# Optimization experiments

Measured on AMD Instinct MI355X. Metric: run time of the kernel, lower is better.

## Reference

```python
import jax, jax.numpy as jnp
import numpy as np

B, S, E = 2, 2048, 2048
H, D = 16, 128
I = 8192
EPS = 1e-5


def layernorm(x, w, b):
    mu = jnp.mean(x, axis=-1, keepdims=True)
    var = jnp.mean(jnp.square(x - mu), axis=-1, keepdims=True)
    return (x - mu) * jax.lax.rsqrt(var + EPS) * w + b


def setup_inputs() -> dict:
    key = jax.random.key(0)
    ks = jax.random.split(key, 6)
    s = 0.02
    return {
        "x": jax.random.normal(ks[0], (B, S, E), jnp.float32),
        "ln1_w": jnp.ones((E,), jnp.float32),
        "ln1_b": jnp.zeros((E,), jnp.float32),
        "Wqkv": jax.random.normal(ks[1], (E, 3 * E), jnp.float32) * s,
        "Wo": jax.random.normal(ks[2], (E, E), jnp.float32) * s,
        "ln2_w": jnp.ones((E,), jnp.float32),
        "ln2_b": jnp.zeros((E,), jnp.float32),
        "W1": jax.random.normal(ks[3], (E, I), jnp.float32) * s,
        "W2": jax.random.normal(ks[4], (I, E), jnp.float32) * s,
    }


def reference(x, ln1_w, ln1_b, Wqkv, Wo, ln2_w, ln2_b, W1, W2):
    scale = D ** -0.5
    # --- attention sublayer (pre-LN) ---
    h = layernorm(x, ln1_w, ln1_b)
    qkv = (h @ Wqkv).reshape(B, S, 3, H, D)
    q, k, v = [jnp.moveaxis(qkv[:, :, i], 1, 2) for i in range(3)]  # [B,H,S,D]
    scores = jnp.einsum("bhqd,bhkd->bhqk", q, k) * scale
    causal = jnp.triu(jnp.ones((S, S), bool), k=1)
    scores = jnp.where(causal, -jnp.inf, scores)
    attn = jax.nn.softmax(scores, axis=-1)
    out = jnp.einsum("bhqk,bhkd->bqhd", attn, v).reshape(B, S, E)
    x = x + out @ Wo
    # --- FFN sublayer (pre-LN) ---
    h = layernorm(x, ln2_w, ln2_b)
    x = x + jax.nn.gelu(h @ W1, approximate=True) @ W2
    return x
```

## Files before the change

kernel.cpp:

```cpp
#include <hip/hip_runtime.h>
#include <hip/hip_bf16.h>

#define B_ 2
#define S_ 2048
#define E_ 2048
#define H_ 16
#define D_ 128
#define I_ 8192
#define T_ (B_*S_)

typedef __attribute__((ext_vector_type(8))) short bf16x8;
typedef __attribute__((ext_vector_type(8))) unsigned short us8;
typedef __attribute__((ext_vector_type(4))) float f32x4;

__device__ __forceinline__ unsigned short f2bf(float f) {
  union { float f; unsigned int u; } c; c.f = f;
  unsigned int u = c.u;
  unsigned int r = (u + 0x7fffu + ((u >> 16) & 1u)) >> 16;
  return (unsigned short)r;
}

__device__ __forceinline__ void gload16(const void* g, void* l) {
  __builtin_amdgcn_global_load_lds((const __attribute__((address_space(1))) void*)g,
                                   (__attribute__((address_space(3))) void*)l, 16, 0, 0);
}

__global__ void transpose_w(const float* __restrict__ in, unsigned short* __restrict__ out,
                            int K, int N) {
  __shared__ float tile[32][33];
  const int n0 = blockIdx.x * 32, k0 = blockIdx.y * 32;
  const int tx = threadIdx.x, ty = threadIdx.y;
#pragma unroll
  for (int j = 0; j < 4; ++j) {
    int k = k0 + ty + j * 8;
    tile[ty + j * 8][tx] = in[(size_t)k * N + n0 + tx];
  }
  __syncthreads();
#pragma unroll
  for (int j = 0; j < 4; ++j) {
    int n = n0 + ty + j * 8;
    out[(size_t)n * K + k0 + tx] = f2bf(tile[tx][ty + j * 8]);
  }
}

__global__ void ln_kernel(const float* __restrict__ x, const float* __restrict__ w,
                          const float* __restrict__ b, unsigned short* __restrict__ out) {
  const int row = blockIdx.x;
  const int tid = threadIdx.x;
  const int wid = tid >> 6, lane = tid & 63;
  const float4* xr = (const float4*)(x + (size_t)row * E_);
  float4 v0 = xr[tid * 2], v1 = xr[tid * 2 + 1];
  float s  = v0.x + v0.y + v0.z + v0.w + v1.x + v1.y + v1.z + v1.w;
  float sq = v0.x*v0.x + v0.y*v0.y + v0.z*v0.z + v0.w*v0.w
           + v1.x*v1.x + v1.y*v1.y + v1.z*v1.z + v1.w*v1.w;
#pragma unroll
  for (int off = 32; off > 0; off >>= 1) {
    s  += __shfl_xor(s, off);
    sq += __shfl_xor(sq, off);
  }
  __shared__ float red[8];
  if (lane == 0) { red[wid] = s; red[wid + 4] = sq; }
  __syncthreads();
  s  = red[0] + red[1] + red[2] + red[3];
  sq = red[4] + red[5] + red[6] + red[7];
  const float mu  = s * (1.0f / E_);
  const float var = sq * (1.0f / E_) - mu * mu;
  const float rstd = rsqrtf(var + 1e-5f);
  const float4* w4 = (const float4*)w + tid * 2;
  const float4* b4 = (const float4*)b + tid * 2;
  float4 w0 = w4[0], w1 = w4[1], bb0 = b4[0], bb1 = b4[1];
  us8 o;
  o[0] = f2bf((v0.x - mu) * rstd * w0.x + bb0.x);
  o[1] = f2bf((v0.y - mu) * rstd * w0.y + bb0.y);
  o[2] = f2bf((v0.z - mu) * rstd * w0.z + bb0.z);
  o[3] = f2bf((v0.w - mu) * rstd * w0.w + bb0.w);
  o[4] = f2bf((v1.x - mu) * rstd * w1.x + bb1.x);
  o[5] = f2bf((v1.y - mu) * rstd * w1.y + bb1.y);
  o[6] = f2bf((v1.z - mu) * rstd * w1.z + bb1.z);
  o[7] = f2bf((v1.w - mu) * rstd * w1.w + bb1.w);
  *(us8*)(&out[(size_t)row * E_ + tid * 8]) = o;
}

template<int EPI>
__global__ void gemm_bt(const unsigned short* __restrict__ A,
                        const unsigned short* __restrict__ Bt,
                        void* __restrict__ Cout,
                        const float* __restrict__ resid,
                        int M, int N, int K) {
  __shared__ __align__(16) unsigned short As[128 * 32];
  __shared__ __align__(16) unsigned short Bs[128 * 32];
  const int gn = N >> 7;
  const int nwg = (M >> 7) * gn;
  const int cpx = nwg >> 3;
  const int bid = blockIdx.x;
  const int swz = (bid & 7) * cpx + (bid >> 3);
  const int bm = swz / gn, bn = swz % gn;
  const int tid = threadIdx.x;
  const int wid = tid >> 6, lane = tid & 63;
  const int fr = lane & 15, kg = lane >> 4;
  const int wr = wid >> 1, wc = wid & 1;

  const int c0 = wid * 2;
  const unsigned short* gA = A  + (size_t)(bm * 128 + c0 * 16 + (lane >> 2)) * K + (lane & 3) * 8;
  const unsigned short* gB = Bt + (size_t)(bn * 128 + c0 * 16 + (lane >> 2)) * K + (lane & 3) * 8;
  unsigned short* lA = &As[c0 * 512];
  unsigned short* lB = &Bs[c0 * 512];

  const unsigned short* rA = &As[(wr * 64 + fr) * 32 + kg * 8];
  const unsigned short* rB = &Bs[(wc * 64 + fr) * 32 + kg * 8];

  f32x4 acc[4][4] = {};
  const int nk = K >> 5;
  for (int kt = 0; kt < nk; ++kt) {
    __syncthreads();
    gload16(gA,                 lA);
    gload16(gA + 16 * (size_t)K, lA + 512);
    gload16(gB,                 lB);
    gload16(gB + 16 * (size_t)K, lB + 512);
    gA += 32; gB += 32;
    __syncthreads();
    bf16x8 af[4], bfr[4];
#pragma unroll
    for (int m = 0; m < 4; ++m) af[m]  = *(const bf16x8*)(rA + m * 16 * 32);
#pragma unroll
    for (int n = 0; n < 4; ++n) bfr[n] = *(const bf16x8*)(rB + n * 16 * 32);
#pragma unroll
    for (int m = 0; m < 4; ++m)
#pragma unroll
      for (int n = 0; n < 4; ++n)
        acc[m][n] = __builtin_amdgcn_mfma_f32_16x16x32_bf16(af[m], bfr[n], acc[m][n], 0, 0, 0);
  }

  const int row0 = bm * 128 + wr * 64;
  const int col0 = bn * 128 + wc * 64;
#pragma unroll
  for (int m = 0; m < 4; ++m) {
#pragma unroll
    for (int n = 0; n < 4; ++n) {
#pragma unroll
      for (int r = 0; r < 4; ++r) {
        const int row = row0 + m * 16 + kg * 4 + r;
        const int col = col0 + n * 16 + fr;
        const size_t idx = (size_t)row * N + col;
        const float v = acc[m][n][r];
        if constexpr (EPI == 0) {
          ((unsigned short*)Cout)[idx] = f2bf(v);
        } else if constexpr (EPI == 1) {
          const float u = 0.7978845608028654f * (v + 0.044715f * v * v * v);
          const float gel = 0.5f * v * (1.0f + tanhf(u));
          ((unsigned short*)Cout)[idx] = f2bf(gel);
        } else {
          ((float*)Cout)[idx] = v + resid[idx];
        }
      }
    }
  }
}

__global__ void extract_vT(const unsigned short* __restrict__ qkv, unsigned short* __restrict__ vT) {
  __shared__ unsigned short tile[32][34];
  const int bh = blockIdx.z;
  const int b = bh >> 4, h = bh & 15;
  const int s0 = blockIdx.y * 32, d0 = blockIdx.x * 32;
  const int tx = threadIdx.x, ty = threadIdx.y;
#pragma unroll
  for (int j = 0; j < 4; ++j) {
    int s = s0 + ty + j * 8;
    tile[ty + j * 8][tx] = qkv[(size_t)(b * S_ + s) * 6144 + 4096 + h * 128 + d0 + tx];
  }
  __syncthreads();
#pragma unroll
  for (int j = 0; j < 4; ++j) {
    int d = d0 + ty + j * 8;
    vT[((size_t)bh * 128 + d) * 2048 + s0 + tx] = tile[tx][ty + j * 8];
  }
}

__global__ __launch_bounds__(256, 2)
void attn_kernel(const unsigned short* __restrict__ qkv,
                 const unsigned short* __restrict__ vT,
                 unsigned short* __restrict__ outp) {
  __shared__ __align__(16) unsigned short Ks[64 * 128];
  __shared__ __align__(16) unsigned short Vts[128 * 64];
  __shared__ __align__(16) unsigned short Ps[4 * 16 * 40];
  const int qt = blockIdx.x;
  const int bh = blockIdx.y;
  const int b = bh >> 4, h = bh & 15;
  const int tid = threadIdx.x, wid = tid >> 6, lane = tid & 63;
  const int fr = lane & 15, g = lane >> 4;

  const unsigned short* qptr = qkv + (size_t)(b * S_ + qt * 64 + wid * 16 + fr) * 6144 + h * 128;
  bf16x8 qf[4];
#pragma unroll
  for (int dc = 0; dc < 4; ++dc) qf[dc] = *(const bf16x8*)(qptr + dc * 32 + g * 8);

  float m0[4], l0[4];
#pragma unroll
  for (int r = 0; r < 4; ++r) { m0[r] = -1e30f; l0[r] = 0.0f; }
  f32x4 acc[8] = {};

  const unsigned short* kbase = qkv + (size_t)(b * S_) * 6144 + 2048 + h * 128;
  const unsigned short* vbase = vT + (size_t)bh * 128 * 2048;
  unsigned short* Pw = &Ps[wid * 640];
  const float scale = 0.08838834764831845f;

  us8 kreg[4], vreg[4];
#pragma unroll
  for (int j = 0; j < 4; ++j) {
    const int cc = tid + 256 * j;
    kreg[j] = *(const us8*)(kbase + (size_t)(cc >> 4) * 6144 + (cc & 15) * 8);
    vreg[j] = *(const us8*)(vbase + (size_t)(cc >> 3) * 2048 + (cc & 7) * 8);
  }

  for (int kt = 0; kt <= qt; ++kt) {
    __syncthreads();
#pragma unroll
    for (int j = 0; j < 4; ++j) {
      const int cc = tid + 256 * j;
      const int krow = cc >> 4, kcp = cc & 15;
      *(us8*)(&Ks[krow * 128 + ((kcp * 8) ^ ((krow & 7) << 3))]) = kreg[j];
      const int drow = cc >> 3, vcp = cc & 7;
      *(us8*)(&Vts[drow * 64 + ((vcp * 8) ^ ((drow & 7) << 3))]) = vreg[j];
    }
    if (kt < qt) {
#pragma unroll
      for (int j = 0; j < 4; ++j) {
        const int cc = tid + 256 * j;
        kreg[j] = *(const us8*)(kbase + (size_t)((kt + 1) * 64 + (cc >> 4)) * 6144 + (cc & 15) * 8);
        vreg[j] = *(const us8*)(vbase + (size_t)(cc >> 3) * 2048 + (kt + 1) * 64 + (cc & 7) * 8);
      }
    }
    __syncthreads();

    f32x4 sc[4] = {};
    __builtin_amdgcn_s_setprio(1);
#pragma unroll
    for (int dc = 0; dc < 4; ++dc) {
#pragma unroll
      for (int sub = 0; sub < 4; ++sub) {
        const int row = sub * 16 + fr;
        bf16x8 kf = *(const bf16x8*)(&Ks[row * 128 + ((dc * 32 + g * 8) ^ ((row & 7) << 3))]);
        sc[sub] = __builtin_amdgcn_mfma_f32_16x16x32_bf16(qf[dc], kf, sc[sub], 0, 0, 0);
      }
    }
    __builtin_amdgcn_s_setprio(0);

    float p[4][4];
    const bool diag = (kt == qt);
#pragma unroll
    for (int sub = 0; sub < 4; ++sub) {
#pragma unroll
      for (int r = 0; r < 4; ++r) {
        float v = sc[sub][r] * scale;
        if (diag && (sub * 16 + fr > wid * 16 + g * 4 + r)) v = -1e30f;
        p[sub][r] = v;
      }
    }
    float corr[4];
#pragma unroll
    for (int r = 0; r < 4; ++r) {
      float mx = fmaxf(fmaxf(p[0][r], p[1][r]), fmaxf(p[2][r], p[3][r]));
#pragma unroll
      for (int off = 1; off < 16; off <<= 1) mx = fmaxf(mx, __shfl_xor(mx, off));
      const float mn = fmaxf(m0[r], mx);
      corr[r] = __expf(m0[r] - mn);
      m0[r] = mn;
      float rs = 0.0f;
#pragma unroll
      for (int sub = 0; sub < 4; ++sub) { p[sub][r] = __expf(p[sub][r] - mn); rs += p[sub][r]; }
#pragma unroll
      for (int off = 1; off < 16; off <<= 1) rs += __shfl_xor(rs, off);
      l0[r] = l0[r] * corr[r] + rs;
    }
#pragma unroll
    for (int dt = 0; dt < 8; ++dt)
#pragma unroll
      for (int r = 0; r < 4; ++r) acc[dt][r] *= corr[r];

#pragma unroll
    for (int half = 0; half < 2; ++half) {
#pragma unroll
      for (int s2 = 0; s2 < 2; ++s2)
#pragma unroll
        for (int r = 0; r < 4; ++r)
          Pw[(g * 4 + r) * 40 + s2 * 16 + fr] = f2bf(p[half * 2 + s2][r]);
      bf16x8 pf = *(const bf16x8*)(&Pw[fr * 40 + g * 8]);
      __builtin_amdgcn_s_setprio(1);
#pragma unroll
      for (int dt = 0; dt < 8; ++dt) {
        const int row = dt * 16 + fr;
        bf16x8 vf = *(const bf16x8*)(&Vts[row * 64 + ((half * 32 + g * 8) ^ ((row & 7) << 3))]);
        acc[dt] = __builtin_amdgcn_mfma_f32_16x16x32_bf16(pf, vf, acc[dt], 0, 0, 0);
      }
      __builtin_amdgcn_s_setprio(0);
    }
  }

  float inv[4];
#pragma unroll
  for (int r = 0; r < 4; ++r) inv[r] = 1.0f / l0[r];
#pragma unroll
  for (int dt = 0; dt < 8; ++dt)
#pragma unroll
    for (int r = 0; r < 4; ++r) {
      const size_t row = (size_t)(b * S_ + qt * 64 + wid * 16 + g * 4 + r);
      outp[row * E_ + h * 128 + dt * 16 + fr] = f2bf(acc[dt][r] * inv[r]);
    }
}

extern "C" void kernel_launch(void* const* d_in, const int* in_sizes, int n_in,
                              void* d_out, int out_size, void* d_ws, size_t ws_size,
                              hipStream_t stream) {
  (void)in_sizes; (void)n_in; (void)out_size; (void)ws_size;
  const float* x    = (const float*)d_in[0];
  const float* ln1w = (const float*)d_in[1];
  const float* ln1b = (const float*)d_in[2];
  const float* Wqkv = (const float*)d_in[3];
  const float* Wo   = (const float*)d_in[4];
  const float* ln2w = (const float*)d_in[5];
  const float* ln2b = (const float*)d_in[6];
  const float* W1   = (const float*)d_in[7];
  const float* W2   = (const float*)d_in[8];
  float* out = (float*)d_out;
  char* ws = (char*)d_ws;

  unsigned short* WqkvT = (unsigned short*)(ws + 0);
  unsigned short* WoT   = (unsigned short*)(ws + 25165824);
  unsigned short* W1T   = (unsigned short*)(ws + 33554432);
  unsigned short* W2T   = (unsigned short*)(ws + 67108864);
  unsigned short* qkvb  = (unsigned short*)(ws + 100663296);
  unsigned short* vTb   = (unsigned short*)(ws + 150994944);
  unsigned short* gbuf  = (unsigned short*)(ws + 100663296);
  unsigned short* hbuf  = (unsigned short*)(ws + 167772160);
  float*          x1    = (float*)         (ws + 184549376);

  const dim3 tb(32, 8);
  hipLaunchKernelGGL(transpose_w, dim3(6144 / 32, 2048 / 32), tb, 0, stream, Wqkv, WqkvT, 2048, 6144);
  hipLaunchKernelGGL(transpose_w, dim3(2048 / 32, 2048 / 32), tb, 0, stream, Wo,   WoT,   2048, 2048);
  hipLaunchKernelGGL(transpose_w, dim3(8192 / 32, 2048 / 32), tb, 0, stream, W1,   W1T,   2048, 8192);
  hipLaunchKernelGGL(transpose_w, dim3(2048 / 32, 8192 / 32), tb, 0, stream, W2,   W2T,   8192, 2048);

  hipLaunchKernelGGL(ln_kernel, dim3(T_), dim3(256), 0, stream, x, ln1w, ln1b, hbuf);
  hipLaunchKernelGGL((gemm_bt<0>), dim3(32 * 48), dim3(256), 0, stream,
                     hbuf, WqkvT, (void*)qkvb, (const float*)nullptr, T_, 6144, 2048);
  hipLaunchKernelGGL(extract_vT, dim3(4, 64, 32), tb, 0, stream, qkvb, vTb);
  hipLaunchKernelGGL(attn_kernel, dim3(S_ / 64, B_ * H_), dim3(256), 0, stream, qkvb, vTb, hbuf);
  hipLaunchKernelGGL((gemm_bt<2>), dim3(32 * 16), dim3(256), 0, stream,
                     hbuf, WoT, (void*)x1, x, T_, 2048, 2048);
  hipLaunchKernelGGL(ln_kernel, dim3(T_), dim3(256), 0, stream, x1, ln2w, ln2b, hbuf);
  hipLaunchKernelGGL((gemm_bt<1>), dim3(32 * 64), dim3(256), 0, stream,
                     hbuf, W1T, (void*)gbuf, (const float*)nullptr, T_, 8192, 2048);
  hipLaunchKernelGGL((gemm_bt<2>), dim3(32 * 16), dim3(256), 0, stream,
                     gbuf, W2T, (void*)out, x1, T_, 2048, 8192);
}
```

Measured before the change: 797.5 us.

## Replace 128x128 GEMM with double-buffered 256x256 tile pipelined kernel

Replaces the simple 128x128 single-buffered GEMM with a 256x256 tile, 512-thread kernel. It double-buffers LDS across K-steps, interleaves global-to-LDS prefetch with MFMA phases, and uses an XOR-swizzled LDS layout to avoid bank conflicts. The goal is to raise arithmetic intensity and hide global load latency behind MFMAs. In exchange it uses 128KB of LDS and many more accumulator registers, and for the Wo/W2 GEMMs it launches only 128 workgroups, which may underfill the CUs.

```diff
diff --git a/kernel.cpp b/kernel.cpp
--- a/kernel.cpp
+++ b/kernel.cpp
@@ -82,59 +82,111 @@
 }
 
 template<int EPI>
-__global__ void gemm_bt(const unsigned short* __restrict__ A,
-                        const unsigned short* __restrict__ Bt,
-                        void* __restrict__ Cout,
-                        const float* __restrict__ resid,
-                        int M, int N, int K) {
-  __shared__ __align__(16) unsigned short As[128 * 32];
-  __shared__ __align__(16) unsigned short Bs[128 * 32];
-  const int gn = N >> 7;
-  const int nwg = (M >> 7) * gn;
+__global__ __launch_bounds__(512, 2)
+void gemm256(const unsigned short* __restrict__ A,
+             const unsigned short* __restrict__ Bt,
+             void* __restrict__ Cout,
+             const float* __restrict__ resid,
+             int M, int N, int K) {
+  __shared__ __align__(16) unsigned short lds[65536];
+  const int gn = N >> 8;
+  const int nwg = (M >> 8) * gn;
   const int cpx = nwg >> 3;
   const int bid = blockIdx.x;
   const int swz = (bid & 7) * cpx + (bid >> 3);
   const int bm = swz / gn, bn = swz % gn;
   const int tid = threadIdx.x;
-  const int wid = tid >> 6, lane = tid & 63;
+  const int w = tid >> 6, lane = tid & 63;
   const int fr = lane & 15, kg = lane >> 4;
-  const int wr = wid >> 1, wc = wid & 1;
-
-  const int c0 = wid * 2;
-  const unsigned short* gA = A  + (size_t)(bm * 128 + c0 * 16 + (lane >> 2)) * K + (lane & 3) * 8;
-  const unsigned short* gB = Bt + (size_t)(bn * 128 + c0 * 16 + (lane >> 2)) * K + (lane & 3) * 8;
-  unsigned short* lA = &As[c0 * 512];
-  unsigned short* lB = &Bs[c0 * 512];
-
-  const unsigned short* rA = &As[(wr * 64 + fr) * 32 + kg * 8];
-  const unsigned short* rB = &Bs[(wc * 64 + fr) * 32 + kg * 8];
-
-  f32x4 acc[4][4] = {};
-  const int nk = K >> 5;
+  const int wr = w >> 2, wc = w & 3;
+
+  const int cc_s = (tid & 7) ^ ((tid >> 3) & 7);
+  const int row_s = 2 * (tid >> 3) + (cc_s >> 2);
+  const int ks_s = (cc_s & 3) * 8;
+  const unsigned short* gA = A  + (size_t)(bm * 256 + row_s) * K + ks_s;
+  const unsigned short* gB = Bt + (size_t)(bn * 256 + row_s) * K + ks_s;
+
+  const int lread = (fr >> 1) * 64 + ((((fr & 1) * 4 + kg) ^ (fr >> 1)) * 8);
+
+  auto STG = [&](const unsigned short* g, unsigned short* l) {
+    gload16(g, l);
+    gload16(g + (size_t)128 * K, l + 4096);
+  };
+#define REG_(op, c, kh) (((((op) * 2 + (c)) * 2 + (kh))) * 8192)
+
+  f32x4 acc[8][4] = {};
+  bf16x8 af[4], bq[4];
+
+  auto LDA4 = [&](int c, int kh, int mh) {
+    const unsigned short* p = &lds[REG_(0, c, kh) + (wr * 64 + mh * 32) * 64 + lread];
+#pragma unroll
+    for (int m = 0; m < 4; ++m) af[m] = *(const bf16x8*)(p + m * 512);
+  };
+  auto LDB4 = [&](int c, int kh) {
+    const unsigned short* p = &lds[REG_(1, c, kh) + (wc * 32) * 64 + lread];
+#pragma unroll
+    for (int n = 0; n < 4; ++n) bq[n] = *(const bf16x8*)(p + n * 512);
+  };
+  auto MM16 = [&](int mh) {
+    __builtin_amdgcn_s_setprio(1);
+#pragma unroll
+    for (int m = 0; m < 4; ++m)
+#pragma unroll
+      for (int n = 0; n < 4; ++n)
+        acc[mh * 4 + m][n] =
+            __builtin_amdgcn_mfma_f32_16x16x32_bf16(af[m], bq[n], acc[mh * 4 + m][n], 0, 0, 0);
+    __builtin_amdgcn_s_setprio(0);
+  };
+
+  const int nk = K >> 6;
+  STG(gA,      &lds[REG_(0, 0, 0) + w * 512]);
+  STG(gB,      &lds[REG_(1, 0, 0) + w * 512]);
+  STG(gA + 32, &lds[REG_(0, 0, 1) + w * 512]);
+  STG(gB + 32, &lds[REG_(1, 0, 1) + w * 512]);
+  asm volatile("s_waitcnt vmcnt(4)" ::: "memory");
+  __builtin_amdgcn_s_barrier();
+
   for (int kt = 0; kt < nk; ++kt) {
-    __syncthreads();
-    gload16(gA,                 lA);
-    gload16(gA + 16 * (size_t)K, lA + 512);
-    gload16(gB,                 lB);
-    gload16(gB + 16 * (size_t)K, lB + 512);
-    gA += 32; gB += 32;
-    __syncthreads();
-    bf16x8 af[4], bfr[4];
-#pragma unroll
-    for (int m = 0; m < 4; ++m) af[m]  = *(const bf16x8*)(rA + m * 16 * 32);
-#pragma unroll
-    for (int n = 0; n < 4; ++n) bfr[n] = *(const bf16x8*)(rB + n * 16 * 32);
-#pragma unroll
-    for (int m = 0; m < 4; ++m)
-#pragma unroll
-      for (int n = 0; n < 4; ++n)
-        acc[m][n] = __builtin_amdgcn_mfma_f32_16x16x32_bf16(af[m], bfr[n], acc[m][n], 0, 0, 0);
-  }
-
-  const int row0 = bm * 128 + wr * 64;
-  const int col0 = bn * 128 + wc * 64;
-#pragma unroll
-  for (int m = 0; m < 4; ++m) {
+    const int c = kt & 1, d = c ^ 1;
+    const bool pf = (kt + 1 < nk);
+    const int knext = (kt + 1) * 64;
+    LDA4(c, 0, 0); LDB4(c, 0);
+    if (pf) STG(gA + knext, &lds[REG_(0, d, 0) + w * 512]);
+    __builtin_amdgcn_s_barrier();
+    asm volatile("s_waitcnt lgkmcnt(0)" ::: "memory");
+    __builtin_amdgcn_sched_barrier(0);
+    MM16(0);
+    __builtin_amdgcn_s_barrier();
+    LDA4(c, 0, 1);
+    if (pf) STG(gB + knext, &lds[REG_(1, d, 0) + w * 512]);
+    __builtin_amdgcn_s_barrier();
+    asm volatile("s_waitcnt lgkmcnt(0)" ::: "memory");
+    __builtin_amdgcn_sched_barrier(0);
+    MM16(1);
+    if (pf) asm volatile("s_waitcnt vmcnt(4)" ::: "memory");
+    else    asm volatile("s_waitcnt vmcnt(0)" ::: "memory");
+    __builtin_amdgcn_s_barrier();
+    LDA4(c, 1, 0); LDB4(c, 1);
+    if (pf) STG(gA + knext + 32, &lds[REG_(0, d, 1) + w * 512]);
+    __builtin_amdgcn_s_barrier();
+    asm volatile("s_waitcnt lgkmcnt(0)" ::: "memory");
+    __builtin_amdgcn_sched_barrier(0);
+    MM16(0);
+    __builtin_amdgcn_s_barrier();
+    LDA4(c, 1, 1);
+    if (pf) STG(gB + knext + 32, &lds[REG_(1, d, 1) + w * 512]);
+    __builtin_amdgcn_s_barrier();
+    asm volatile("s_waitcnt lgkmcnt(0)" ::: "memory");
+    __builtin_amdgcn_sched_barrier(0);
+    MM16(1);
+    if (pf) asm volatile("s_waitcnt vmcnt(4)" ::: "memory");
+    __builtin_amdgcn_s_barrier();
+  }
+
+  const int row0 = bm * 256 + wr * 128;
+  const int col0 = bn * 256 + wc * 64;
+#pragma unroll
+  for (int m = 0; m < 8; ++m) {
 #pragma unroll
     for (int n = 0; n < 4; ++n) {
 #pragma unroll
@@ -155,6 +207,7 @@
       }
     }
   }
+#undef REG_
 }
 
 __global__ void extract_vT(const unsigned short* __restrict__ qkv, unsigned short* __restrict__ vT) {
@@ -341,15 +394,15 @@
   hipLaunchKernelGGL(transpose_w, dim3(2048 / 32, 8192 / 32), tb, 0, stream, W2,   W2T,   8192, 2048);
 
   hipLaunchKernelGGL(ln_kernel, dim3(T_), dim3(256), 0, stream, x, ln1w, ln1b, hbuf);
-  hipLaunchKernelGGL((gemm_bt<0>), dim3(32 * 48), dim3(256), 0, stream,
+  hipLaunchKernelGGL((gemm256<0>), dim3(16 * 24), dim3(512), 0, stream,
                      hbuf, WqkvT, (void*)qkvb, (const float*)nullptr, T_, 6144, 2048);
   hipLaunchKernelGGL(extract_vT, dim3(4, 64, 32), tb, 0, stream, qkvb, vTb);
   hipLaunchKernelGGL(attn_kernel, dim3(S_ / 64, B_ * H_), dim3(256), 0, stream, qkvb, vTb, hbuf);
-  hipLaunchKernelGGL((gemm_bt<2>), dim3(32 * 16), dim3(256), 0, stream,
+  hipLaunchKernelGGL((gemm256<2>), dim3(16 * 8), dim3(512), 0, stream,
                      hbuf, WoT, (void*)x1, x, T_, 2048, 2048);
   hipLaunchKernelGGL(ln_kernel, dim3(T_), dim3(256), 0, stream, x1, ln2w, ln2b, hbuf);
-  hipLaunchKernelGGL((gemm_bt<1>), dim3(32 * 64), dim3(256), 0, stream,
+  hipLaunchKernelGGL((gemm256<1>), dim3(16 * 32), dim3(512), 0, stream,
                      hbuf, W1T, (void*)gbuf, (const float*)nullptr, T_, 8192, 2048);
-  hipLaunchKernelGGL((gemm_bt<2>), dim3(32 * 16), dim3(256), 0, stream,
+  hipLaunchKernelGGL((gemm256<2>), dim3(16 * 8), dim3(512), 0, stream,
                      gbuf, W2T, (void*)out, x1, T_, 2048, 8192);
 }
```

Measured after the change: 827.7 us. +3.8%, slower.

## Add 256x256-tile 8-wave GEMM with interleaved prefetch for FFN up-projection

Applied to the files above, without the earlier changes.

Adds a new GEMM kernel with 256x256 output tiles, 512 threads, double-buffered LDS filled by direct global-to-LDS loads, a swizzled LDS layout, and inline ds_read with manual waitcnt/barrier scheduling and MFMA priority bumps. It is used only for the W1 GEMM with GELU epilogue. The larger tile raises operand reuse and cuts global traffic per FLOP. In exchange it needs more registers and LDS, launches fewer workgroups (512), and relies on a fragile hand-built sync schedule.

```diff
diff --git a/kernel.cpp b/kernel.cpp
--- a/kernel.cpp
+++ b/kernel.cpp
@@ -157,6 +157,141 @@
   }
 }
 
+#define DSR(dst, addr, off) \
+  asm volatile("ds_read_b128 %0, %1 offset:%c2" : "=v"(dst) : "v"(addr), "i"(off))
+#define LDA4_(aad, kh, mh) \
+  DSR(af[0], aad, (kh)*16384 + (mh)*4096 + 0);    \
+  DSR(af[1], aad, (kh)*16384 + (mh)*4096 + 1024); \
+  DSR(af[2], aad, (kh)*16384 + (mh)*4096 + 2048); \
+  DSR(af[3], aad, (kh)*16384 + (mh)*4096 + 3072)
+#define LDB4_(bbd, kh) \
+  DSR(bq[0], bbd, (kh)*16384 + 0);    \
+  DSR(bq[1], bbd, (kh)*16384 + 1024); \
+  DSR(bq[2], bbd, (kh)*16384 + 2048); \
+  DSR(bq[3], bbd, (kh)*16384 + 3072)
+#define FENCE_ do { asm volatile("s_waitcnt lgkmcnt(0)"); \
+                    __builtin_amdgcn_sched_barrier(0); } while (0)
+#define REG_(op, c, kh) (((((op) * 2 + (c)) * 2 + (kh))) * 8192)
+
+template<int EPI>
+__global__ __launch_bounds__(512, 2)
+void gemm256(const unsigned short* __restrict__ A,
+             const unsigned short* __restrict__ Bt,
+             void* __restrict__ Cout,
+             const float* __restrict__ resid,
+             int M, int N, int K) {
+  __shared__ __align__(16) unsigned short lds[65536];
+  const int gn = N >> 8;
+  const int nwg = (M >> 8) * gn;
+  const int cpx = nwg >> 3;
+  const int bid = blockIdx.x;
+  const int swz = (bid & 7) * cpx + (bid >> 3);
+  const int bm = swz / gn, bn = swz % gn;
+  const int tid = threadIdx.x;
+  const int w = tid >> 6, lane = tid & 63;
+  const int fr = lane & 15, kg = lane >> 4;
+  const int wr = w >> 2, wc = w & 3;
+
+  const int cc_s = (tid & 7) ^ ((tid >> 3) & 7);
+  const int row_s = 2 * (tid >> 3) + (cc_s >> 2);
+  const int ks_s = (cc_s & 3) * 8;
+  const unsigned short* gA = A  + (size_t)(bm * 256 + row_s) * K + ks_s;
+  const unsigned short* gB = Bt + (size_t)(bn * 256 + row_s) * K + ks_s;
+
+  const int lread = (fr >> 1) * 64 + ((((fr & 1) * 4 + kg) ^ (fr >> 1)) * 8);
+  const int aA0 = wr * 8192 + lread * 2;
+  const int aA1 = 32768 + wr * 8192 + lread * 2;
+  const int bB0 = 65536 + wc * 4096 + lread * 2;
+  const int bB1 = 65536 + 32768 + wc * 4096 + lread * 2;
+
+  auto STG = [&](const unsigned short* g, unsigned short* l) {
+    gload16(g, l);
+    gload16(g + (size_t)128 * K, l + 4096);
+  };
+
+  f32x4 acc[8][4] = {};
+  bf16x8 af[4], bq[4];
+
+  auto MM16 = [&](int mh) {
+    __builtin_amdgcn_s_setprio(1);
+#pragma unroll
+    for (int m = 0; m < 4; ++m)
+#pragma unroll
+      for (int n = 0; n < 4; ++n)
+        acc[mh * 4 + m][n] =
+            __builtin_amdgcn_mfma_f32_16x16x32_bf16(af[m], bq[n], acc[mh * 4 + m][n], 0, 0, 0);
+    __builtin_amdgcn_s_setprio(0);
+  };
+
+#define KTILE(AAD, BBD, DB, kt)  {                                        \
+    const bool pf = (kt) + 1 < nk;                                        \
+    const unsigned short* gAn = gA + (size_t)((kt) + 1) * 64;             \
+    const unsigned short* gBn = gB + (size_t)((kt) + 1) * 64;             \
+    LDA4_(AAD, 0, 0); LDB4_(BBD, 0);                                      \
+    if (pf) STG(gAn, &lds[REG_(0, DB, 0) + w * 512]);                     \
+    __builtin_amdgcn_s_barrier(); FENCE_;                                 \
+    MM16(0);                                                              \
+    __builtin_amdgcn_s_barrier();                                         \
+    LDA4_(AAD, 0, 1);                                                     \
+    if (pf) STG(gBn, &lds[REG_(1, DB, 0) + w * 512]);                     \
+    __builtin_amdgcn_s_barrier(); FENCE_;                                 \
+    MM16(1);                                                              \
+    if (pf) { asm volatile("s_waitcnt vmcnt(4)" ::: "memory"); }          \
+    else    { asm volatile("s_waitcnt vmcnt(0)" ::: "memory"); }          \
+    __builtin_amdgcn_s_barrier();                                         \
+    LDA4_(AAD, 1, 0); LDB4_(BBD, 1);                                      \
+    if (pf) STG(gAn + 32, &lds[REG_(0, DB, 1) + w * 512]);                \
+    __builtin_amdgcn_s_barrier(); FENCE_;                                 \
+    MM16(0);                                                              \
+    __builtin_amdgcn_s_barrier();                                         \
+    LDA4_(AAD, 1, 1);                                                     \
+    if (pf) STG(gBn + 32, &lds[REG_(1, DB, 1) + w * 512]);                \
+    __builtin_amdgcn_s_barrier(); FENCE_;                                 \
+    MM16(1);                                                              \
+    if (pf) { asm volatile("s_waitcnt vmcnt(4)" ::: "memory"); }          \
+    __builtin_amdgcn_s_barrier();                                         \
+  }
+
+  const int nk = K >> 6;
+  STG(gA,      &lds[REG_(0, 0, 0) + w * 512]);
+  STG(gB,      &lds[REG_(1, 0, 0) + w * 512]);
+  STG(gA + 32, &lds[REG_(0, 0, 1) + w * 512]);
+  STG(gB + 32, &lds[REG_(1, 0, 1) + w * 512]);
+  asm volatile("s_waitcnt vmcnt(4)" ::: "memory");
+  __builtin_amdgcn_s_barrier();
+
+  for (int kt2 = 0; kt2 < (nk >> 1); ++kt2) {
+    KTILE(aA0, bB0, 1, 2 * kt2);
+    KTILE(aA1, bB1, 0, 2 * kt2 + 1);
+  }
+#undef KTILE
+
+  const int row0 = bm * 256 + wr * 128;
+  const int col0 = bn * 256 + wc * 64;
+#pragma unroll
+  for (int m = 0; m < 8; ++m) {
+#pragma unroll
+    for (int n = 0; n < 4; ++n) {
+#pragma unroll
+      for (int r = 0; r < 4; ++r) {
+        const int row = row0 + m * 16 + kg * 4 + r;
+        const int col = col0 + n * 16 + fr;
+        const size_t idx = (size_t)row * N + col;
+        const float v = acc[m][n][r];
+        if constexpr (EPI == 0) {
+          ((unsigned short*)Cout)[idx] = f2bf(v);
+        } else if constexpr (EPI == 1) {
+          const float u = 0.7978845608028654f * (v + 0.044715f * v * v * v);
+          const float gel = 0.5f * v * (1.0f + tanhf(u));
+          ((unsigned short*)Cout)[idx] = f2bf(gel);
+        } else {
+          ((float*)Cout)[idx] = v + resid[idx];
+        }
+      }
+    }
+  }
+}
+
 __global__ void extract_vT(const unsigned short* __restrict__ qkv, unsigned short* __restrict__ vT) {
   __shared__ unsigned short tile[32][34];
   const int bh = blockIdx.z;
@@ -348,7 +483,7 @@
   hipLaunchKernelGGL((gemm_bt<2>), dim3(32 * 16), dim3(256), 0, stream,
                      hbuf, WoT, (void*)x1, x, T_, 2048, 2048);
   hipLaunchKernelGGL(ln_kernel, dim3(T_), dim3(256), 0, stream, x1, ln2w, ln2b, hbuf);
-  hipLaunchKernelGGL((gemm_bt<1>), dim3(32 * 64), dim3(256), 0, stream,
+  hipLaunchKernelGGL((gemm256<1>), dim3(16 * 32), dim3(512), 0, stream,
                      hbuf, W1T, (void*)gbuf, (const float*)nullptr, T_, 8192, 2048);
   hipLaunchKernelGGL((gemm_bt<2>), dim3(32 * 16), dim3(256), 0, stream,
                      gbuf, W2T, (void*)out, x1, T_, 2048, 8192);
```

Measured after the change: 766.3 us. -3.9%, faster.

## Use 32x32x16 bf16 MFMA GEMM kernel for the FFN matmuls

Applied to the files above, without the earlier changes.

Adds a new GEMM kernel, gemm32, that uses 32x32x16 bf16 MFMA instructions, an XOR-swizzled LDS layout, direct global-to-LDS loads, an XCD-aware block swizzle and launch bounds allowing 3 blocks per CU. It is used only for the two FFN GEMMs, W1 with fused GELU and W2 with fused residual. The larger MFMA shape is meant to cut LDS reads per FLOP and raise matrix-core throughput for these large matmuls. The K loop loads and syncs once per 64-wide slice with no double buffering, and the scalar epilogue stores may be poorly coalesced.

```diff
diff --git a/kernel.cpp b/kernel.cpp
--- a/kernel.cpp
+++ b/kernel.cpp
@@ -12,6 +12,7 @@
 typedef __attribute__((ext_vector_type(8))) short bf16x8;
 typedef __attribute__((ext_vector_type(8))) unsigned short us8;
 typedef __attribute__((ext_vector_type(4))) float f32x4;
+typedef __attribute__((ext_vector_type(16))) float f32x16;
 
 __device__ __forceinline__ unsigned short f2bf(float f) {
   union { float f; unsigned int u; } c; c.f = f;
@@ -157,6 +158,86 @@
   }
 }
 
+template<int EPI>
+__global__ __launch_bounds__(256, 3)
+void gemm32(const unsigned short* __restrict__ A,
+            const unsigned short* __restrict__ Bt,
+            void* __restrict__ Cout,
+            const float* __restrict__ resid,
+            int M, int N, int K) {
+  __shared__ __align__(16) unsigned short As[128 * 64];
+  __shared__ __align__(16) unsigned short Bs[128 * 64];
+  const int gn = N >> 7;
+  const int nwg = (M >> 7) * gn;
+  const int cpx = nwg >> 3;
+  const int bid = blockIdx.x;
+  const int swz = (bid & 7) * cpx + (bid >> 3);
+  const int bm = swz / gn, bn = swz % gn;
+  const int tid = threadIdx.x;
+  const int wid = tid >> 6, lane = tid & 63;
+  const int wr = wid >> 1, wc = wid & 1;
+  const int r31 = lane & 31, hi = lane >> 5;
+  const int rsw = r31 & 7;
+
+  const int trow = tid >> 3;
+  const int tc = (tid & 7) ^ (trow & 7);
+  const unsigned short* gA = A  + (size_t)(bm * 128 + trow) * K + tc * 8;
+  const unsigned short* gB = Bt + (size_t)(bn * 128 + trow) * K + tc * 8;
+  unsigned short* lA = &As[tid * 8];
+  unsigned short* lB = &Bs[tid * 8];
+
+  f32x16 acc[2][2] = {};
+  const int nk = K >> 6;
+  for (int kt = 0; kt < nk; ++kt) {
+    __syncthreads();
+#pragma unroll
+    for (int s = 0; s < 4; ++s) {
+      gload16(gA + (size_t)(s * 32) * K, lA + s * 2048);
+      gload16(gB + (size_t)(s * 32) * K, lB + s * 2048);
+    }
+    gA += 64; gB += 64;
+    __syncthreads();
+#pragma unroll
+    for (int ks = 0; ks < 4; ++ks) {
+      const int ca = ((ks * 2 + hi) ^ rsw) * 8;
+      bf16x8 a0 = *(const bf16x8*)(&As[(wr * 64 +      r31) * 64 + ca]);
+      bf16x8 a1 = *(const bf16x8*)(&As[(wr * 64 + 32 + r31) * 64 + ca]);
+      bf16x8 b0 = *(const bf16x8*)(&Bs[(wc * 64 +      r31) * 64 + ca]);
+      bf16x8 b1 = *(const bf16x8*)(&Bs[(wc * 64 + 32 + r31) * 64 + ca]);
+      acc[0][0] = __builtin_amdgcn_mfma_f32_32x32x16_bf16(a0, b0, acc[0][0], 0, 0, 0);
+      acc[0][1] = __builtin_amdgcn_mfma_f32_32x32x16_bf16(a0, b1, acc[0][1], 0, 0, 0);
+      acc[1][0] = __builtin_amdgcn_mfma_f32_32x32x16_bf16(a1, b0, acc[1][0], 0, 0, 0);
+      acc[1][1] = __builtin_amdgcn_mfma_f32_32x32x16_bf16(a1, b1, acc[1][1], 0, 0, 0);
+    }
+  }
+
+  const int row0 = bm * 128 + wr * 64;
+  const int col0 = bn * 128 + wc * 64;
+#pragma unroll
+  for (int mt = 0; mt < 2; ++mt) {
+#pragma unroll
+    for (int nt = 0; nt < 2; ++nt) {
+#pragma unroll
+      for (int rg = 0; rg < 16; ++rg) {
+        const int rl = (rg & 3) + 8 * (rg >> 2) + 4 * hi;
+        const int row = row0 + mt * 32 + rl;
+        const int col = col0 + nt * 32 + r31;
+        const size_t idx = (size_t)row * N + col;
+        const float v = acc[mt][nt][rg];
+        if constexpr (EPI == 0) {
+          ((unsigned short*)Cout)[idx] = f2bf(v);
+        } else if constexpr (EPI == 1) {
+          const float u = 0.7978845608028654f * (v + 0.044715f * v * v * v);
+          const float gel = 0.5f * v * (1.0f + tanhf(u));
+          ((unsigned short*)Cout)[idx] = f2bf(gel);
+        } else {
+          ((float*)Cout)[idx] = v + resid[idx];
+        }
+      }
+    }
+  }
+}
+
 __global__ void extract_vT(const unsigned short* __restrict__ qkv, unsigned short* __restrict__ vT) {
   __shared__ unsigned short tile[32][34];
   const int bh = blockIdx.z;
@@ -348,8 +429,8 @@
   hipLaunchKernelGGL((gemm_bt<2>), dim3(32 * 16), dim3(256), 0, stream,
                      hbuf, WoT, (void*)x1, x, T_, 2048, 2048);
   hipLaunchKernelGGL(ln_kernel, dim3(T_), dim3(256), 0, stream, x1, ln2w, ln2b, hbuf);
-  hipLaunchKernelGGL((gemm_bt<1>), dim3(32 * 64), dim3(256), 0, stream,
+  hipLaunchKernelGGL((gemm32<1>), dim3(32 * 64), dim3(256), 0, stream,
                      hbuf, W1T, (void*)gbuf, (const float*)nullptr, T_, 8192, 2048);
-  hipLaunchKernelGGL((gemm_bt<2>), dim3(32 * 16), dim3(256), 0, stream,
+  hipLaunchKernelGGL((gemm32<2>), dim3(32 * 16), dim3(256), 0, stream,
                      gbuf, W2T, (void*)out, x1, T_, 2048, 8192);
 }
```

After: 788.4 us. Within noise of the previous version (-1.1%).
